# Optimization experiments

Hardware: AMD Instinct MI355X
Metric: run time of the kernel (lower is better)

The kernel has to match this reference:

```python
import jax, jax.numpy as jnp
from jax import lax
import numpy as np

VOCAB = 100000
MAX_SEQ = 8192
DIM = 128
K = 5
STRIDE = 1
PAD = 2


def setup_inputs() -> dict:
    key = jax.random.key(0)
    ks = jax.random.split(key, 6)
    X = jax.random.randint(ks[0], (8, 8192), 0, VOCAB, dtype=jnp.int64)
    # nn.Linear(vocab, dim): weight (dim, vocab), bias (dim)
    W_lin = jax.random.normal(ks[1], (DIM, VOCAB), dtype=jnp.float32) * 0.02
    b_lin = jax.random.normal(ks[2], (DIM,), dtype=jnp.float32) * 0.02
    # nn.Conv1d(dim, dim, k): weight (out=dim, in=dim, k), bias (dim)
    W_conv = jax.random.normal(ks[3], (DIM, DIM, K), dtype=jnp.float32) * 0.02
    b_conv = jax.random.normal(ks[4], (DIM,), dtype=jnp.float32) * 0.02
    # nn.Embedding(max_seq_len, dim)
    pos_table = jax.random.normal(ks[5], (MAX_SEQ, DIM), dtype=jnp.float32) * 0.02
    return {"X": X, "W_lin": W_lin, "b_lin": b_lin,
            "W_conv": W_conv, "b_conv": b_conv, "pos_table": pos_table}


def reference(X, W_lin, b_lin, W_conv, b_conv, pos_table):
    # one_hot(X) @ W_lin.T + b_lin  ==  gather rows of W_lin.T
    emb = jnp.take(W_lin.T, X, axis=0) + b_lin          # (b, n, d)
    x = jnp.transpose(emb, (0, 2, 1))                   # (b, d, n)
    y = lax.conv_general_dilated(
        x, W_conv, window_strides=(STRIDE,), padding=[(PAD, PAD)],
        dimension_numbers=("NCH", "OIH", "NCH"))
    y = y + b_conv[None, :, None]                       # (b, d, n_out)
    tokens = jnp.transpose(y, (0, 2, 1))                # (b, n_out, d)
    n_out = tokens.shape[1]
    return tokens + pos_table[:n_out][None, :, :]
```

## Files before the change

### kernel.cpp

```cpp
#include <hip/hip_runtime.h>
#include <hip/hip_bf16.h>
#include <stdint.h>

#define VOCAB 100000
#define SEQ   8192
#define BATCH 8
#define DIM   128

typedef short bf16x8 __attribute__((ext_vector_type(8)));
typedef float f32x4  __attribute__((ext_vector_type(4)));

__device__ __forceinline__ ushort f2bf(float f) {
  union { float f; uint32_t u; } v; v.f = f;
  uint32_t u = v.u;
  return (ushort)((u + 0x7FFF + ((u >> 16) & 1)) >> 16);
}

__global__ void repack_wconv(const float* __restrict__ wconv,
                             ushort* __restrict__ wcb) {
  int e = blockIdx.x * 256 + threadIdx.x;
  if (e >= 5 * DIM * DIM) return;
  int k = e / (DIM * DIM);
  int rem = e % (DIM * DIM);
  int d = rem / DIM, i = rem % DIM;
  wcb[e] = f2bf(wconv[(d * DIM + i) * 5 + k]);
}

__global__ __launch_bounds__(256) void build_wlt(
    const float* __restrict__ wlin, const float* __restrict__ blin,
    ushort* __restrict__ wlt) {
  __shared__ float tile[128 * 65];
  const int tid = threadIdx.x;
  const int t0  = blockIdx.x * 64;

  const int c4 = (tid & 15) * 4;
  const int rbase = tid >> 4;
  const bool cvalid = (t0 + c4) < VOCAB;
#pragma unroll
  for (int p = 0; p < 8; ++p) {
    int r = p * 16 + rbase;
    float4 v = make_float4(0.f, 0.f, 0.f, 0.f);
    if (cvalid) v = *(const float4*)(wlin + (size_t)r * VOCAB + t0 + c4);
    float* dst = &tile[r * 65 + c4];
    dst[0] = v.x; dst[1] = v.y; dst[2] = v.z; dst[3] = v.w;
  }
  __syncthreads();

  const int chunk = tid & 15;
  float bias8[8];
#pragma unroll
  for (int j = 0; j < 8; ++j) bias8[j] = blin[chunk * 8 + j];

#pragma unroll
  for (int p = 0; p < 4; ++p) {
    int tl = (tid >> 4) + p * 16;
    int t  = t0 + tl;
    if (t >= VOCAB) continue;
    ushort u[8];
#pragma unroll
    for (int j = 0; j < 8; ++j) {
      float f = tile[(chunk * 8 + j) * 65 + tl] + bias8[j];
      u[j] = f2bf(f);
    }
    *(uint4*)(wlt + (size_t)t * DIM + chunk * 8) = *(const uint4*)u;
  }
}

__global__ __launch_bounds__(256, 2) void conv_main(
    const int* __restrict__ X, const ushort* __restrict__ wlt,
    const ushort* __restrict__ wcb, const float* __restrict__ bconv,
    const float* __restrict__ pos, float* __restrict__ out) {
  __shared__ __align__(16) ushort Atile[132 * 136];

  const int tid   = threadIdx.x;
  const int bm    = blockIdx.x;
  const int batch = bm >> 6;
  const int nbase = (bm & 63) << 7;
  const int* Xb   = X + batch * SEQ;

  int  tok[9];
  bool valid[9];
#pragma unroll
  for (int it = 0; it < 9; ++it) {
    int c = tid + it * 256;
    int r = c >> 4;
    int n = nbase - 2 + r;
    bool v = (c < 2112) && (n >= 0) && (n < SEQ);
    valid[it] = v;
    tok[it] = v ? Xb[n] : 0;
  }
  uint4 val[9];
#pragma unroll
  for (int it = 0; it < 9; ++it) {
    int c = tid + it * 256;
    int ch = c & 15;
    val[it] = valid[it] ? *(const uint4*)(wlt + (size_t)tok[it] * DIM + ch * 8)
                        : make_uint4(0u, 0u, 0u, 0u);
  }
#pragma unroll
  for (int it = 0; it < 9; ++it) {
    int c = tid + it * 256;
    if (c < 2112) {
      int r = c >> 4, ch = c & 15;
      *(uint4*)&Atile[r * 136 + ch * 8] = val[it];
    }
  }
  __syncthreads();

  const int wave = tid >> 6;
  const int lane = tid & 63;
  const int wm = (wave >> 1) << 6;
  const int wn = (wave & 1) << 6;
  const int lr = lane & 15;
  const int lq = lane >> 4;

  f32x4 acc[4][4];
#pragma unroll
  for (int a = 0; a < 4; ++a)
#pragma unroll
    for (int b = 0; b < 4; ++b) acc[a][b] = (f32x4)0.f;

#pragma unroll
  for (int k = 0; k < 5; ++k) {
    bf16x8 B[4][4];
#pragma unroll
    for (int nt = 0; nt < 4; ++nt)
#pragma unroll
      for (int kk = 0; kk < 4; ++kk)
        B[nt][kk] = *(const bf16x8*)(wcb +
            ((size_t)(k * DIM + wn + nt * 16 + lr) * DIM + kk * 32 + lq * 8));
#pragma unroll
    for (int kk = 0; kk < 4; ++kk) {
      bf16x8 A[4];
#pragma unroll
      for (int mt = 0; mt < 4; ++mt)
        A[mt] = *(const bf16x8*)&Atile[(wm + mt * 16 + lr + k) * 136 + kk * 32 + lq * 8];
#pragma unroll
      for (int mt = 0; mt < 4; ++mt)
#pragma unroll
        for (int nt = 0; nt < 4; ++nt)
          acc[mt][nt] = __builtin_amdgcn_mfma_f32_16x16x32_bf16(
              A[mt], B[nt][kk], acc[mt][nt], 0, 0, 0);
    }
  }

  float bc[4];
#pragma unroll
  for (int nt = 0; nt < 4; ++nt) bc[nt] = bconv[wn + nt * 16 + lr];
  float* outb = out + (size_t)batch * SEQ * DIM;
#pragma unroll
  for (int mt = 0; mt < 4; ++mt) {
#pragma unroll
    for (int rr = 0; rr < 4; ++rr) {
      int m = wm + mt * 16 + lq * 4 + rr;
      int gn = nbase + m;
      const float* posrow = pos + (size_t)gn * DIM;
      float* orow = outb + (size_t)gn * DIM;
#pragma unroll
      for (int nt = 0; nt < 4; ++nt) {
        int d = wn + nt * 16 + lr;
        orow[d] = acc[mt][nt][rr] + bc[nt] + posrow[d];
      }
    }
  }
}

extern "C" void kernel_launch(void* const* d_in, const int* in_sizes, int n_in,
                              void* d_out, int out_size, void* d_ws, size_t ws_size,
                              hipStream_t stream) {
  const int*   X     = (const int*)d_in[0];
  const float* wlin  = (const float*)d_in[1];
  const float* blin  = (const float*)d_in[2];
  const float* wconv = (const float*)d_in[3];
  const float* bconv = (const float*)d_in[4];
  const float* pos   = (const float*)d_in[5];
  float*       out   = (float*)d_out;

  ushort* wcb = (ushort*)d_ws;
  ushort* wlt = (ushort*)((char*)d_ws + 262144);

  hipLaunchKernelGGL(repack_wconv, dim3(320), dim3(256), 0, stream, wconv, wcb);
  hipLaunchKernelGGL(build_wlt, dim3((VOCAB + 63) / 64), dim3(256), 0, stream,
                     wlin, blin, wlt);
  hipLaunchKernelGGL(conv_main, dim3(512), dim3(256), 0, stream,
                     X, wlt, wcb, bconv, pos, out);
}
```

Baseline: 143.7 us.

## Merge table-build kernels and transpose MFMA output for vectorized epilogue stores

Folds the conv-weight repack into the vocab table-building kernel as extra blocks, which removes one kernel launch. In the conv kernel the MFMA operands are swapped so each lane holds four consecutive output channels. The epilogue can then use 16-byte vector loads of bias and positional rows and 16-byte nontemporal stores instead of scalar strided accesses. The output write pattern changes to per-row float4, and nontemporal stores bypass cache retention.

```diff
diff --git a/kernel.cpp b/kernel.cpp
--- a/kernel.cpp
+++ b/kernel.cpp
@@ -6,6 +6,7 @@
 #define SEQ   8192
 #define BATCH 8
 #define DIM   128
+#define NB_WLT 1563
 
 typedef short bf16x8 __attribute__((ext_vector_type(8)));
 typedef float f32x4  __attribute__((ext_vector_type(4)));
@@ -16,22 +17,28 @@
   return (ushort)((u + 0x7FFF + ((u >> 16) & 1)) >> 16);
 }
 
-__global__ void repack_wconv(const float* __restrict__ wconv,
-                             ushort* __restrict__ wcb) {
-  int e = blockIdx.x * 256 + threadIdx.x;
-  if (e >= 5 * DIM * DIM) return;
-  int k = e / (DIM * DIM);
-  int rem = e % (DIM * DIM);
-  int d = rem / DIM, i = rem % DIM;
-  wcb[e] = f2bf(wconv[(d * DIM + i) * 5 + k]);
-}
-
-__global__ __launch_bounds__(256) void build_wlt(
+__global__ __launch_bounds__(256) void build_tables(
     const float* __restrict__ wlin, const float* __restrict__ blin,
-    ushort* __restrict__ wlt) {
+    const float* __restrict__ wconv, ushort* __restrict__ wlt,
+    ushort* __restrict__ wcb) {
   __shared__ float tile[128 * 65];
   const int tid = threadIdx.x;
-  const int t0  = blockIdx.x * 64;
+
+  if (blockIdx.x >= NB_WLT) {
+    int e = (blockIdx.x - NB_WLT) * 1024 + tid;
+#pragma unroll
+    for (int i = 0; i < 4; ++i, e += 256) {
+      if (e < 5 * DIM * DIM) {
+        int k = e >> 14;
+        int rem = e & 16383;
+        int d = rem >> 7, ii = rem & 127;
+        wcb[e] = f2bf(wconv[(d * DIM + ii) * 5 + k]);
+      }
+    }
+    return;
+  }
+
+  const int t0 = blockIdx.x * 64;
 
   const int c4 = (tid & 15) * 4;
   const int rbase = tid >> 4;
@@ -140,27 +147,21 @@
 #pragma unroll
         for (int nt = 0; nt < 4; ++nt)
           acc[mt][nt] = __builtin_amdgcn_mfma_f32_16x16x32_bf16(
-              A[mt], B[nt][kk], acc[mt][nt], 0, 0, 0);
+              B[nt][kk], A[mt], acc[mt][nt], 0, 0, 0);
     }
   }
 
-  float bc[4];
-#pragma unroll
-  for (int nt = 0; nt < 4; ++nt) bc[nt] = bconv[wn + nt * 16 + lr];
   float* outb = out + (size_t)batch * SEQ * DIM;
 #pragma unroll
-  for (int mt = 0; mt < 4; ++mt) {
+  for (int nt = 0; nt < 4; ++nt) {
+    int d0 = wn + nt * 16 + lq * 4;
+    const f32x4 bc4 = *(const f32x4*)(bconv + d0);
 #pragma unroll
-    for (int rr = 0; rr < 4; ++rr) {
-      int m = wm + mt * 16 + lq * 4 + rr;
-      int gn = nbase + m;
-      const float* posrow = pos + (size_t)gn * DIM;
-      float* orow = outb + (size_t)gn * DIM;
-#pragma unroll
-      for (int nt = 0; nt < 4; ++nt) {
-        int d = wn + nt * 16 + lr;
-        orow[d] = acc[mt][nt][rr] + bc[nt] + posrow[d];
-      }
+    for (int mt = 0; mt < 4; ++mt) {
+      int gn = nbase + wm + mt * 16 + lr;
+      const f32x4 p4 = *(const f32x4*)(pos + (size_t)gn * DIM + d0);
+      f32x4 v = acc[mt][nt] + bc4 + p4;
+      __builtin_nontemporal_store(v, (f32x4*)(outb + (size_t)gn * DIM + d0));
     }
   }
 }
@@ -179,9 +180,8 @@
   ushort* wcb = (ushort*)d_ws;
   ushort* wlt = (ushort*)((char*)d_ws + 262144);
 
-  hipLaunchKernelGGL(repack_wconv, dim3(320), dim3(256), 0, stream, wconv, wcb);
-  hipLaunchKernelGGL(build_wlt, dim3((VOCAB + 63) / 64), dim3(256), 0, stream,
-                     wlin, blin, wlt);
+  hipLaunchKernelGGL(build_tables, dim3(NB_WLT + 80), dim3(256), 0, stream,
+                     wlin, blin, wconv, wlt, wcb);
   hipLaunchKernelGGL(conv_main, dim3(512), dim3(256), 0, stream,
                      X, wlt, wcb, bconv, pos, out);
 }
```

Result: slower. 148.2 us (+3.2%).
